# Performance work log

Measured on AMD Instinct MI355X. Metric: run time of the kernel, lower is better.

Reference implementation:

```python
import jax, jax.numpy as jnp
import numpy as np

N_NODES = 50000
N_EDGES = 800000
N_RELS = 65
D = 64
N_GRAPHS = 512


def setup_inputs() -> dict:
    key = jax.random.key(0)
    ks = jax.random.split(key, 20)
    inp = {
        "node_feats": jax.random.normal(ks[0], (N_NODES, D), dtype=jnp.float32),
        "etypes": jax.random.randint(ks[1], (N_EDGES,), 0, N_RELS),
        "src": jax.random.randint(ks[2], (N_EDGES,), 0, N_NODES),
        "dst": jax.random.randint(ks[3], (N_EDGES,), 0, N_NODES),
        "graph_ids": jnp.sort(jax.random.randint(ks[4], (N_NODES,), 0, N_GRAPHS)),
    }
    s = 1.0 / np.sqrt(D)
    # 3 RGCN layers: per-relation weights (basis with num_bases=num_rels == full) + bias
    for i, k in zip(range(1, 4), (ks[5], ks[6], ks[7])):
        inp[f"W_rel{i}"] = jax.random.normal(k, (N_RELS, D, D), dtype=jnp.float32) * s
        inp[f"b{i}"] = jnp.zeros((D,), dtype=jnp.float32)
    # 3 FC layers
    for i, k in zip(range(1, 4), (ks[8], ks[9], ks[10])):
        inp[f"fc_W{i}"] = jax.random.normal(k, (D, D), dtype=jnp.float32) * s
        inp[f"fc_b{i}"] = jnp.zeros((D,), dtype=jnp.float32)
    inp["pred_W"] = jax.random.normal(ks[11], (D, 2), dtype=jnp.float32) * s
    inp["pred_b"] = jnp.zeros((2,), dtype=jnp.float32)
    return inp


def _rgcn_layer(h, W, b, etypes, src, dst):
    # all-relation projection: [N, R, K]
    proj = jnp.einsum('nd,rdk->nrk', h, W)
    # per-edge gather of relation-specific message: [E, K]
    msg = proj[src, etypes]
    # scatter-sum into destination nodes
    agg = jax.ops.segment_sum(msg, dst, num_segments=h.shape[0])
    return jax.nn.relu(agg + b)


def reference(node_feats, etypes, src, dst, graph_ids,
              W_rel1, b1, W_rel2, b2, W_rel3, b3,
              fc_W1, fc_b1, fc_W2, fc_b2, fc_W3, fc_b3,
              pred_W, pred_b):
    h = node_feats
    h = _rgcn_layer(h, W_rel1, b1, etypes, src, dst)
    h = _rgcn_layer(h, W_rel2, b2, etypes, src, dst)
    h = _rgcn_layer(h, W_rel3, b3, etypes, src, dst)
    # sum-pool nodes per graph: [G, D]
    g = jax.ops.segment_sum(h, graph_ids, num_segments=N_GRAPHS)
    g = jax.nn.relu(g @ fc_W1 + fc_b1)
    g = jax.nn.relu(g @ fc_W2 + fc_b2)
    g = jax.nn.relu(g @ fc_W3 + fc_b3)
    return g @ pred_W + pred_b
```

## Files before the change

kernel.cpp:

```cpp
#include <hip/hip_runtime.h>
#include <hip/hip_bf16.h>

#define N_NODES 50000
#define N_EDGES 800000
#define N_RELS 65
#define DIM 64
#define N_GRAPHS 512

#define SORT_BLOCKS 1024
#define CHUNK ((N_EDGES + SORT_BLOCKS - 1) / SORT_BLOCKS)

#define SCAN_BLK 512
#define NSCAN_BLKS ((N_NODES + SCAN_BLK - 1) / SCAN_BLK)

#define MSG_BLOCKS 2048
#define NWAVES (MSG_BLOCKS * 4)

typedef __attribute__((ext_vector_type(8))) short short8;
typedef __attribute__((ext_vector_type(4))) float f32x4;


__global__ __launch_bounds__(256) void prep_kernel(
    const float* __restrict__ x, const int* __restrict__ et,
    __hip_bfloat16* __restrict__ y, int* __restrict__ cnt_d,
    int* __restrict__ blk_hist,
    const float* __restrict__ W1, const float* __restrict__ W2,
    const float* __restrict__ W3,
    __hip_bfloat16* __restrict__ Wt1, __hip_bfloat16* __restrict__ Wt2,
    __hip_bfloat16* __restrict__ Wt3,
    int* __restrict__ done_flags) {
    __shared__ int lh[N_RELS];
    __shared__ float tile[64][65];
    int t = threadIdx.x, b = blockIdx.x;
    int gtid = b * 256 + t;

    if (gtid < N_NODES) cnt_d[gtid] = 0;
    if (gtid < 2) done_flags[gtid] = 0;

    if (t < N_RELS) lh[t] = 0;
    __syncthreads();
    int lo = b * CHUNK;
    int hi = lo + CHUNK; if (hi > N_EDGES) hi = N_EDGES;
    for (int i = lo + t; i < hi; i += 256)
        atomicAdd(&lh[et[i]], 1);

    for (int i = gtid; i < (N_NODES * DIM) / 4; i += SORT_BLOCKS * 256) {
        float4 v = *(const float4*)(x + (size_t)i * 4);
        unsigned short us[4];
        us[0] = __hip_bfloat16_raw(__float2bfloat16(v.x)).x;
        us[1] = __hip_bfloat16_raw(__float2bfloat16(v.y)).x;
        us[2] = __hip_bfloat16_raw(__float2bfloat16(v.z)).x;
        us[3] = __hip_bfloat16_raw(__float2bfloat16(v.w)).x;
        *(ushort4*)(y + (size_t)i * 4) = *(const ushort4*)us;
    }

    if (b < 3 * N_RELS) {
        int which = b / N_RELS, r = b - which * N_RELS;
        const float* W = (which == 0) ? W1 : (which == 1) ? W2 : W3;
        __hip_bfloat16* Wt = (which == 0) ? Wt1 : (which == 1) ? Wt2 : Wt3;
        for (int i = t; i < 4096; i += 256) {
            int row = i >> 6, col = i & 63;
            tile[row][col] = W[(size_t)r * 4096 + i];
        }
        __syncthreads();
        for (int i = t; i < 4096; i += 256) {
            int row = i >> 6, col = i & 63;
            Wt[(size_t)r * 4096 + i] = __float2bfloat16(tile[col][row]);
        }
    }

    __syncthreads();
    if (t < N_RELS) blk_hist[t * SORT_BLOCKS + b] = lh[t];
}


__global__ __launch_bounds__(256) void relscan_kernel(const int* __restrict__ blk_hist,
                                                      int* __restrict__ blk_off,
                                                      int* __restrict__ rel_tot,
                                                      int* __restrict__ rel_ptr,
                                                      int* __restrict__ tile_base,
                                                      int* __restrict__ done) {
    __shared__ int wsum[4];
    int r = blockIdx.x;
    int t = threadIdx.x;
    int w = t >> 6, lane = t & 63;
    const int PER = SORT_BLOCKS / 256;
    int4 v0 = *(const int4*)(blk_hist + (size_t)r * SORT_BLOCKS + t * PER);
    int vals[4] = {v0.x, v0.y, v0.z, v0.w};
    int s = 0;
    #pragma unroll
    for (int j = 0; j < PER; ++j) s += vals[j];
    int x = s;
    #pragma unroll
    for (int off = 1; off < 64; off <<= 1) {
        int y = __shfl_up(x, off);
        if (lane >= off) x += y;
    }
    if (lane == 63) wsum[w] = x;
    __syncthreads();
    int base = 0;
    for (int i = 0; i < w; ++i) base += wsum[i];
    int run = base + x - s;
    int out[4];
    #pragma unroll
    for (int j = 0; j < PER; ++j) { out[j] = run; run += vals[j]; }
    *(int4*)(blk_off + (size_t)r * SORT_BLOCKS + t * PER) = *(const int4*)&out[0];

    if (t == 255) {
        __hip_atomic_store(&rel_tot[r], base + x, __ATOMIC_RELAXED, __HIP_MEMORY_SCOPE_AGENT);
        __threadfence();
        int ticket = atomicAdd(done, 1);
        if (ticket == N_RELS - 1) {
            int ss = 0, tt = 0;
            for (int q = 0; q < N_RELS; ++q) {
                int v = __hip_atomic_load(&rel_tot[q], __ATOMIC_RELAXED,
                                          __HIP_MEMORY_SCOPE_AGENT);
                rel_ptr[q] = ss; ss += v;
                tile_base[q] = tt; tt += (v + 15) >> 4;
            }
            rel_ptr[N_RELS] = N_EDGES;
            tile_base[N_RELS] = tt;
        }
    }
}


__global__ __launch_bounds__(256) void scatter2_kernel(
    const int* __restrict__ et, const int* __restrict__ src,
    const int* __restrict__ dst, const int* __restrict__ blk_hist,
    const int* __restrict__ blk_off, const int* __restrict__ rel_ptr,
    unsigned long long* __restrict__ epk, int* __restrict__ cnt_d) {
    __shared__ unsigned long long buf[CHUNK];
    __shared__ unsigned char relof[CHUNK];
    __shared__ int loff[N_RELS + 1];
    __shared__ int lcur[N_RELS];
    __shared__ int gbase[N_RELS];
    int t = threadIdx.x, b = blockIdx.x;

    if (t < 64) {
        int v = blk_hist[t * SORT_BLOCKS + b];
        int x = v;
        #pragma unroll
        for (int off = 1; off < 64; off <<= 1) {
            int y = __shfl_up(x, off);
            if (t >= off) x += y;
        }
        loff[t] = x - v;
        lcur[t] = x - v;
        gbase[t] = rel_ptr[t] + blk_off[t * SORT_BLOCKS + b];
        if (t == 63) { loff[64] = x; lcur[64] = x; }
    } else if (t == 64) {
        gbase[64] = rel_ptr[64] + blk_off[64 * SORT_BLOCKS + b];
    }
    __syncthreads();

    int lo = b * CHUNK;
    int hi = lo + CHUNK; if (hi > N_EDGES) hi = N_EDGES;
    int nloc = hi - lo;

    #pragma unroll
    for (int k = 0; k < 4; ++k) {
        int i = lo + t + k * 256;
        if (i < hi) {
            int r = et[i], d = dst[i];
            unsigned s = (unsigned)src[i];
            int rank = atomicAdd(&cnt_d[d], 1);
            int pl = atomicAdd(&lcur[r], 1);
            unsigned lo32 = s | ((unsigned)d << 16);
            buf[pl] = (unsigned long long)lo32 |
                      ((unsigned long long)(unsigned)rank << 32);
            relof[pl] = (unsigned char)r;
        }
    }
    __syncthreads();

    #pragma unroll
    for (int k = 0; k < 4; ++k) {
        int i = t + k * 256;
        if (i < nloc) {
            int r = relof[i];
            epk[gbase[r] + i - loff[r]] = buf[i];
        }
    }
}


__global__ __launch_bounds__(SCAN_BLK) void scanblk_kernel(
    const int* __restrict__ cnt, int* __restrict__ outv,
    int* __restrict__ blk_tot, int* __restrict__ blk_base,
    const int* __restrict__ gid, int* __restrict__ g_ptr,
    int* __restrict__ cnt_g, int* __restrict__ done) {
    __shared__ int tmp[SCAN_BLK];
    __shared__ int is_last;
    int t = threadIdx.x;
    int i = blockIdx.x * SCAN_BLK + t;
    int v = (i < N_NODES) ? cnt[i] : 0;
    tmp[t] = v;
    __syncthreads();
    for (int off = 1; off < SCAN_BLK; off <<= 1) {
        int add = (t >= off) ? tmp[t - off] : 0;
        __syncthreads();
        tmp[t] += add;
        __syncthreads();
    }
    if (i < N_NODES) outv[i] = tmp[t] - v;
    if (t == SCAN_BLK - 1) {
        __hip_atomic_store(&blk_tot[blockIdx.x], tmp[t], __ATOMIC_RELAXED,
                           __HIP_MEMORY_SCOPE_AGENT);
        __threadfence();
        int ticket = atomicAdd(done, 1);
        is_last = (ticket == NSCAN_BLKS - 1) ? 1 : 0;
    }
    __syncthreads();
    if (is_last) {
        if (t == 0) {
            int run = 0;
            for (int b2 = 0; b2 < NSCAN_BLKS; ++b2) {
                int v2 = __hip_atomic_load(&blk_tot[b2], __ATOMIC_RELAXED,
                                           __HIP_MEMORY_SCOPE_AGENT);
                blk_base[b2] = run; run += v2;
            }
        }
        if (t < N_GRAPHS) {
            int g = t;
            int lo2 = 0, hi2 = N_NODES;
            while (lo2 < hi2) { int m = (lo2 + hi2) >> 1; if (gid[m] < g) lo2 = m + 1; else hi2 = m; }
            int a2 = lo2;
            lo2 = 0; hi2 = N_NODES;
            int g1 = g + 1;
            while (lo2 < hi2) { int m = (lo2 + hi2) >> 1; if (gid[m] < g1) lo2 = m + 1; else hi2 = m; }
            g_ptr[g] = a2;
            cnt_g[g] = lo2 - a2;
        }
    }
}


__device__ inline unsigned pack2bf(float x, float y) {
    unsigned short ux = __hip_bfloat16_raw(__float2bfloat16(x)).x;
    unsigned short uy = __hip_bfloat16_raw(__float2bfloat16(y)).x;
    return (unsigned)ux | ((unsigned)uy << 16);
}

__global__ __launch_bounds__(256) void msg_mfma_kernel(
    const __hip_bfloat16* __restrict__ hb, const __hip_bfloat16* __restrict__ Wt,
    const int* __restrict__ rel_ptr, const int* __restrict__ tile_base,
    const unsigned long long* __restrict__ epk, const int* __restrict__ outv,
    const int* __restrict__ blk_base,
    __hip_bfloat16* __restrict__ msg) {
    int t = threadIdx.x;
    int w = t >> 6, lane = t & 63;
    int quad = lane >> 4, m16 = lane & 15;
    int wave = blockIdx.x * 4 + w;

    int ntiles = tile_base[N_RELS];
    int tpw = (ntiles + NWAVES - 1) / NWAVES;
    int T = wave * tpw;
    int T1 = T + tpw; if (T1 > ntiles) T1 = ntiles;
    if (T >= T1) return;

    int r = 0;
    while (T >= tile_base[r + 1]) ++r;

    while (T < T1) {
        int chunk_end = tile_base[r + 1]; if (chunk_end > T1) chunk_end = T1;
        int e_base = rel_ptr[r], t_base = tile_base[r];
        int seg_end = rel_ptr[r + 1];

        const __hip_bfloat16* Wr = Wt + (size_t)r * (DIM * DIM);
        short8 bf00 = *(const short8*)(Wr + (4 * m16)     * DIM + quad * 8);
        short8 bf01 = *(const short8*)(Wr + (4 * m16 + 1) * DIM + quad * 8);
        short8 bf02 = *(const short8*)(Wr + (4 * m16 + 2) * DIM + quad * 8);
        short8 bf03 = *(const short8*)(Wr + (4 * m16 + 3) * DIM + quad * 8);
        short8 bf10 = *(const short8*)(Wr + (4 * m16)     * DIM + 32 + quad * 8);
        short8 bf11 = *(const short8*)(Wr + (4 * m16 + 1) * DIM + 32 + quad * 8);
        short8 bf12 = *(const short8*)(Wr + (4 * m16 + 2) * DIM + 32 + quad * 8);
        short8 bf13 = *(const short8*)(Wr + (4 * m16 + 3) * DIM + 32 + quad * 8);

        auto loadidx = [&](int TT, int& sv, int& dp) {
            int TC = TT < chunk_end ? TT : chunk_end - 1;
            int i = e_base + (TC - t_base) * 16 + lane;
            if (i >= N_EDGES) i = N_EDGES - 1;
            unsigned long long e = epk[i];
            int d = (int)((e >> 16) & 0xFFFFu);
            sv = (int)(e & 0xFFFFu);
            dp = (int)(e >> 32) + outv[d] + blk_base[d >> 9];
        };
        auto gatherA = [&](int sv, short8& x0, short8& x1) {
            int s = __shfl(sv, m16);
            const __hip_bfloat16* hp = hb + (size_t)s * DIM + quad * 8;
            x0 = *(const short8*)hp;
            x1 = *(const short8*)(hp + 32);
        };

        int sv0, dp0, sv1, dp1, sv2, dp2;
        short8 a0c, a1c, a0n, a1n;
        loadidx(T,     sv0, dp0);
        loadidx(T + 1, sv1, dp1);
        gatherA(sv0, a0c, a1c);

        for (; T < chunk_end; ++T) {
            loadidx(T + 2, sv2, dp2);
            gatherA(sv1, a0n, a1n);

            int e0 = e_base + (T - t_base) * 16;
            int rows = seg_end - e0; if (rows > 16) rows = 16;

            f32x4 c0 = {0.f, 0.f, 0.f, 0.f}, c1 = c0, c2 = c0, c3 = c0;
            c0 = __builtin_amdgcn_mfma_f32_16x16x32_bf16(a0c, bf00, c0, 0, 0, 0);
            c1 = __builtin_amdgcn_mfma_f32_16x16x32_bf16(a0c, bf01, c1, 0, 0, 0);
            c2 = __builtin_amdgcn_mfma_f32_16x16x32_bf16(a0c, bf02, c2, 0, 0, 0);
            c3 = __builtin_amdgcn_mfma_f32_16x16x32_bf16(a0c, bf03, c3, 0, 0, 0);
            c0 = __builtin_amdgcn_mfma_f32_16x16x32_bf16(a1c, bf10, c0, 0, 0, 0);
            c1 = __builtin_amdgcn_mfma_f32_16x16x32_bf16(a1c, bf11, c1, 0, 0, 0);
            c2 = __builtin_amdgcn_mfma_f32_16x16x32_bf16(a1c, bf12, c2, 0, 0, 0);
            c3 = __builtin_amdgcn_mfma_f32_16x16x32_bf16(a1c, bf13, c3, 0, 0, 0);

            int dpr[4];
            #pragma unroll
            for (int g = 0; g < 4; ++g) dpr[g] = __shfl(dp0, quad * 4 + g);

            #pragma unroll
            for (int g = 0; g < 4; ++g) {
                if (quad * 4 + g < rows) {
                    uint2 pk;
                    pk.x = pack2bf(c0[g], c1[g]);
                    pk.y = pack2bf(c2[g], c3[g]);
                    *(uint2*)(msg + (size_t)dpr[g] * DIM + 4 * m16) = pk;
                }
            }

            sv0 = sv1; dp0 = dp1; sv1 = sv2; dp1 = dp2;
            a0c = a0n; a1c = a1n;
        }
        ++r;
        while (T < T1 && T >= tile_base[r + 1]) ++r;
    }
}


__global__ __launch_bounds__(256) void agg_kernel(
    const __hip_bfloat16* __restrict__ msg, const int* __restrict__ outv,
    const int* __restrict__ blk_base,
    const int* __restrict__ cnt_d, const float* __restrict__ b,
    __hip_bfloat16* __restrict__ hout) {
    int wave = blockIdx.x * 4 + (threadIdx.x >> 6);
    int lane = threadIdx.x & 63;
    if (wave >= N_NODES) return;
    int j0 = outv[wave] + blk_base[wave >> 9];
    int n  = cnt_d[wave];
    int rgrp = lane >> 3, dgrp = lane & 7;

    float a[8] = {0.f, 0.f, 0.f, 0.f, 0.f, 0.f, 0.f, 0.f};
    for (int jj = 0; jj < n; jj += 8) {
        int row = jj + rgrp;
        if (row < n) {
            uint4 d = *(const uint4*)(msg + (size_t)(j0 + row) * DIM + dgrp * 8);
            a[0] += __uint_as_float(d.x << 16);
            a[1] += __uint_as_float(d.x & 0xffff0000u);
            a[2] += __uint_as_float(d.y << 16);
            a[3] += __uint_as_float(d.y & 0xffff0000u);
            a[4] += __uint_as_float(d.z << 16);
            a[5] += __uint_as_float(d.z & 0xffff0000u);
            a[6] += __uint_as_float(d.w << 16);
            a[7] += __uint_as_float(d.w & 0xffff0000u);
        }
    }
    #pragma unroll
    for (int i = 0; i < 8; ++i) {
        a[i] += __shfl_xor(a[i], 8);
        a[i] += __shfl_xor(a[i], 16);
        a[i] += __shfl_xor(a[i], 32);
    }
    if (rgrp == 0) {
        unsigned short us[8];
        #pragma unroll
        for (int i = 0; i < 8; ++i) {
            float v = a[i] + b[dgrp * 8 + i];
            us[i] = __hip_bfloat16_raw(__float2bfloat16(v > 0.f ? v : 0.f)).x;
        }
        *(uint4*)(hout + (size_t)wave * DIM + dgrp * 8) = *(const uint4*)us;
    }
}


__global__ __launch_bounds__(256) void poolfc_kernel(
    const __hip_bfloat16* __restrict__ h, const int* __restrict__ g_ptr,
    const int* __restrict__ cnt_g,
    const float* __restrict__ W1, const float* __restrict__ b1,
    const float* __restrict__ W2, const float* __restrict__ b2,
    const float* __restrict__ W3, const float* __restrict__ b3,
    const float* __restrict__ pW, const float* __restrict__ pb,
    float* __restrict__ out) {
    int wave = blockIdx.x * 4 + (threadIdx.x >> 6);
    int lane = threadIdx.x & 63;
    if (wave >= N_GRAPHS) return;
    int j0 = g_ptr[wave];
    int n  = cnt_g[wave];
    int rgrp = lane >> 3, dgrp = lane & 7;

    float a[8] = {0.f, 0.f, 0.f, 0.f, 0.f, 0.f, 0.f, 0.f};
    for (int jj = 0; jj < n; jj += 8) {
        int row = jj + rgrp;
        if (row < n) {
            uint4 d = *(const uint4*)(h + (size_t)(j0 + row) * DIM + dgrp * 8);
            a[0] += __uint_as_float(d.x << 16);
            a[1] += __uint_as_float(d.x & 0xffff0000u);
            a[2] += __uint_as_float(d.y << 16);
            a[3] += __uint_as_float(d.y & 0xffff0000u);
            a[4] += __uint_as_float(d.z << 16);
            a[5] += __uint_as_float(d.z & 0xffff0000u);
            a[6] += __uint_as_float(d.w << 16);
            a[7] += __uint_as_float(d.w & 0xffff0000u);
        }
    }
    #pragma unroll
    for (int i = 0; i < 8; ++i) {
        a[i] += __shfl_xor(a[i], 8);
        a[i] += __shfl_xor(a[i], 16);
        a[i] += __shfl_xor(a[i], 32);
    }
    float v;
    {
        float acc = b1[lane];
        #pragma unroll
        for (int o = 0; o < 8; ++o)
            #pragma unroll
            for (int q = 0; q < 8; ++q)
                acc += __shfl(a[o], q) * W1[(q * 8 + o) * DIM + lane];
        v = acc > 0.f ? acc : 0.f;
    }
    {
        float acc = b2[lane];
        #pragma unroll
        for (int d = 0; d < DIM; ++d)
            acc += __shfl(v, d) * W2[d * DIM + lane];
        v = acc > 0.f ? acc : 0.f;
    }
    {
        float acc = b3[lane];
        #pragma unroll
        for (int d = 0; d < DIM; ++d)
            acc += __shfl(v, d) * W3[d * DIM + lane];
        v = acc > 0.f ? acc : 0.f;
    }
    float p0 = v * pW[lane * 2 + 0];
    float p1 = v * pW[lane * 2 + 1];
    #pragma unroll
    for (int off = 32; off > 0; off >>= 1) {
        p0 += __shfl_down(p0, off);
        p1 += __shfl_down(p1, off);
    }
    if (lane == 0) {
        out[wave * 2 + 0] = p0 + pb[0];
        out[wave * 2 + 1] = p1 + pb[1];
    }
}


extern "C" void kernel_launch(void* const* d_in, const int* in_sizes, int n_in,
                              void* d_out, int out_size, void* d_ws, size_t ws_size,
                              hipStream_t stream) {
    const float* node_feats = (const float*)d_in[0];
    const int*   etypes     = (const int*)d_in[1];
    const int*   src        = (const int*)d_in[2];
    const int*   dst        = (const int*)d_in[3];
    const int*   graph_ids  = (const int*)d_in[4];
    const float* W1 = (const float*)d_in[5];
    const float* b1 = (const float*)d_in[6];
    const float* W2 = (const float*)d_in[7];
    const float* b2 = (const float*)d_in[8];
    const float* W3 = (const float*)d_in[9];
    const float* b3 = (const float*)d_in[10];
    const float* fcW1 = (const float*)d_in[11];
    const float* fcb1 = (const float*)d_in[12];
    const float* fcW2 = (const float*)d_in[13];
    const float* fcb2 = (const float*)d_in[14];
    const float* fcW3 = (const float*)d_in[15];
    const float* fcb3 = (const float*)d_in[16];
    const float* pW = (const float*)d_in[17];
    const float* pb = (const float*)d_in[18];
    float* out = (float*)d_out;

    char* p = (char*)d_ws;
    auto alloc = [&](size_t bytes) -> void* {
        void* r = (void*)p;
        p += (bytes + 255) & ~(size_t)255;
        return r;
    };
    int* blk_hist  = (int*)alloc((size_t)SORT_BLOCKS * N_RELS * sizeof(int));
    int* blk_off   = (int*)alloc((size_t)SORT_BLOCKS * N_RELS * sizeof(int));
    int* rel_ptr   = (int*)alloc((N_RELS + 1) * sizeof(int));
    int* rel_tot   = (int*)alloc(N_RELS * sizeof(int));
    int* tile_base = (int*)alloc((N_RELS + 1) * sizeof(int));
    unsigned long long* epk = (unsigned long long*)alloc((size_t)N_EDGES * sizeof(unsigned long long));
    int* cnt_d     = (int*)alloc((size_t)N_NODES * sizeof(int));
    int* outv      = (int*)alloc((size_t)N_NODES * sizeof(int));
    int* blk_tot   = (int*)alloc(NSCAN_BLKS * sizeof(int));
    int* blk_base  = (int*)alloc(NSCAN_BLKS * sizeof(int));
    int* cnt_g     = (int*)alloc(N_GRAPHS * sizeof(int));
    int* g_ptr     = (int*)alloc(N_GRAPHS * sizeof(int));
    int* done_flags= (int*)alloc(2 * sizeof(int));
    __hip_bfloat16* hb0 = (__hip_bfloat16*)alloc((size_t)N_NODES * DIM * sizeof(__hip_bfloat16));
    __hip_bfloat16* hb1 = (__hip_bfloat16*)alloc((size_t)N_NODES * DIM * sizeof(__hip_bfloat16));
    __hip_bfloat16* Wt1 = (__hip_bfloat16*)alloc((size_t)N_RELS * DIM * DIM * sizeof(__hip_bfloat16));
    __hip_bfloat16* Wt2 = (__hip_bfloat16*)alloc((size_t)N_RELS * DIM * DIM * sizeof(__hip_bfloat16));
    __hip_bfloat16* Wt3 = (__hip_bfloat16*)alloc((size_t)N_RELS * DIM * DIM * sizeof(__hip_bfloat16));
    __hip_bfloat16* msg = (__hip_bfloat16*)alloc((size_t)N_EDGES * DIM * sizeof(__hip_bfloat16));

    const int AGG_BLOCKS = (N_NODES + 3) / 4;

    prep_kernel<<<SORT_BLOCKS, 256, 0, stream>>>(node_feats, etypes, hb0, cnt_d, blk_hist,
                                                 W1, W2, W3, Wt1, Wt2, Wt3, done_flags);
    relscan_kernel<<<N_RELS, 256, 0, stream>>>(blk_hist, blk_off, rel_tot,
                                               rel_ptr, tile_base, &done_flags[0]);
    scatter2_kernel<<<SORT_BLOCKS, 256, 0, stream>>>(etypes, src, dst, blk_hist, blk_off,
                                                     rel_ptr, epk, cnt_d);
    scanblk_kernel<<<NSCAN_BLKS, SCAN_BLK, 0, stream>>>(cnt_d, outv, blk_tot, blk_base,
                                                        graph_ids, g_ptr, cnt_g,
                                                        &done_flags[1]);

    msg_mfma_kernel<<<MSG_BLOCKS, 256, 0, stream>>>(hb0, Wt1, rel_ptr, tile_base,
                                                    epk, outv, blk_base, msg);
    agg_kernel<<<AGG_BLOCKS, 256, 0, stream>>>(msg, outv, blk_base, cnt_d, b1, hb1);

    msg_mfma_kernel<<<MSG_BLOCKS, 256, 0, stream>>>(hb1, Wt2, rel_ptr, tile_base,
                                                    epk, outv, blk_base, msg);
    agg_kernel<<<AGG_BLOCKS, 256, 0, stream>>>(msg, outv, blk_base, cnt_d, b2, hb0);

    msg_mfma_kernel<<<MSG_BLOCKS, 256, 0, stream>>>(hb0, Wt3, rel_ptr, tile_base,
                                                    epk, outv, blk_base, msg);
    agg_kernel<<<AGG_BLOCKS, 256, 0, stream>>>(msg, outv, blk_base, cnt_d, b3, hb1);

    poolfc_kernel<<<(N_GRAPHS + 3) / 4, 256, 0, stream>>>(hb1, g_ptr, cnt_g,
                                                          fcW1, fcb1, fcW2, fcb2,
                                                          fcW3, fcb3, pW, pb, out);
}
```

Baseline: 391.6 us.

## Replace global atomic dst counting with two-level chunked dst sort then relation scatter

The edge preprocessing now bins edges by destination chunk (512 nodes), sorts each chunk locally in shared memory to build a CSR row_ptr and per-dst counts, then scatters the edges into relation order. The message slot for each edge is therefore its dst-sorted position, so the slot assignment comes from deterministic local sorting rather than per-edge global atomicAdd ranks plus an outv/blk_base lookup. This removes 800k contended global atomics and the extra indirection in msg_mfma and agg. In exchange there are more preprocessing launches and extra passes over the edge arrays.

Result: faster. 369.1 us (-5.8%).

```diff
diff --git a/kernel.cpp b/kernel.cpp
--- a/kernel.cpp
+++ b/kernel.cpp
@@ -7,11 +7,10 @@
 #define DIM 64
 #define N_GRAPHS 512
 
-#define SORT_BLOCKS 1024
-#define CHUNK ((N_EDGES + SORT_BLOCKS - 1) / SORT_BLOCKS)
-
-#define SCAN_BLK 512
-#define NSCAN_BLKS ((N_NODES + SCAN_BLK - 1) / SCAN_BLK)
+#define DCH 512
+#define NCH 98
+#define SB3 256
+#define EC3 3125
 
 #define MSG_BLOCKS 2048
 #define NWAVES (MSG_BLOCKS * 4)
@@ -21,30 +20,32 @@
 
 
 __global__ __launch_bounds__(256) void prep_kernel(
-    const float* __restrict__ x, const int* __restrict__ et,
-    __hip_bfloat16* __restrict__ y, int* __restrict__ cnt_d,
-    int* __restrict__ blk_hist,
+    const float* __restrict__ x, const int* __restrict__ dst,
+    __hip_bfloat16* __restrict__ y, int* __restrict__ blk_hist3,
     const float* __restrict__ W1, const float* __restrict__ W2,
     const float* __restrict__ W3,
     __hip_bfloat16* __restrict__ Wt1, __hip_bfloat16* __restrict__ Wt2,
     __hip_bfloat16* __restrict__ Wt3,
     int* __restrict__ done_flags) {
-    __shared__ int lh[N_RELS];
+    __shared__ int chist[128];
     __shared__ float tile[64][65];
     int t = threadIdx.x, b = blockIdx.x;
     int gtid = b * 256 + t;
 
-    if (gtid < N_NODES) cnt_d[gtid] = 0;
     if (gtid < 2) done_flags[gtid] = 0;
 
-    if (t < N_RELS) lh[t] = 0;
-    __syncthreads();
-    int lo = b * CHUNK;
-    int hi = lo + CHUNK; if (hi > N_EDGES) hi = N_EDGES;
-    for (int i = lo + t; i < hi; i += 256)
-        atomicAdd(&lh[et[i]], 1);
-
-    for (int i = gtid; i < (N_NODES * DIM) / 4; i += SORT_BLOCKS * 256) {
+    if (b < SB3) {
+        if (t < 128) chist[t] = 0;
+        __syncthreads();
+        int lo = b * EC3;
+        #pragma unroll
+        for (int k = 0; k < 13; ++k) {
+            int i = lo + t + k * 256;
+            if (i < lo + EC3) atomicAdd(&chist[dst[i] >> 9], 1);
+        }
+    }
+
+    for (int i = gtid; i < (N_NODES * DIM) / 4; i += 1024 * 256) {
         float4 v = *(const float4*)(x + (size_t)i * 4);
         unsigned short us[4];
         us[0] = __hip_bfloat16_raw(__float2bfloat16(v.x)).x;
@@ -54,8 +55,9 @@
         *(ushort4*)(y + (size_t)i * 4) = *(const ushort4*)us;
     }
 
-    if (b < 3 * N_RELS) {
-        int which = b / N_RELS, r = b - which * N_RELS;
+    if (b >= SB3 && b < SB3 + 3 * N_RELS) {
+        int bb = b - SB3;
+        int which = bb / N_RELS, r = bb - which * N_RELS;
         const float* W = (which == 0) ? W1 : (which == 1) ? W2 : W3;
         __hip_bfloat16* Wt = (which == 0) ? Wt1 : (which == 1) ? Wt2 : Wt3;
         for (int i = t; i < 4096; i += 256) {
@@ -69,28 +71,25 @@
         }
     }
 
-    __syncthreads();
-    if (t < N_RELS) blk_hist[t * SORT_BLOCKS + b] = lh[t];
-}
-
-
-__global__ __launch_bounds__(256) void relscan_kernel(const int* __restrict__ blk_hist,
-                                                      int* __restrict__ blk_off,
-                                                      int* __restrict__ rel_tot,
-                                                      int* __restrict__ rel_ptr,
-                                                      int* __restrict__ tile_base,
-                                                      int* __restrict__ done) {
+    if (b < SB3) {
+        __syncthreads();
+        if (t < NCH) blk_hist3[t * SB3 + b] = chist[t];
+    }
+}
+
+
+__global__ __launch_bounds__(256) void chunkscan_kernel(
+    const int* __restrict__ blk_hist3, int* __restrict__ blk_off3,
+    int* __restrict__ chunk_tot, int* __restrict__ chunk_ptr,
+    const int* __restrict__ gid, int* __restrict__ g_ptr, int* __restrict__ cnt_g,
+    int* __restrict__ done) {
     __shared__ int wsum[4];
-    int r = blockIdx.x;
-    int t = threadIdx.x;
+    __shared__ int is_last;
+    int r = blockIdx.x, t = threadIdx.x;
     int w = t >> 6, lane = t & 63;
-    const int PER = SORT_BLOCKS / 256;
-    int4 v0 = *(const int4*)(blk_hist + (size_t)r * SORT_BLOCKS + t * PER);
-    int vals[4] = {v0.x, v0.y, v0.z, v0.w};
-    int s = 0;
-    #pragma unroll
-    for (int j = 0; j < PER; ++j) s += vals[j];
-    int x = s;
+
+    int v = blk_hist3[r * SB3 + t];
+    int x = v;
     #pragma unroll
     for (int off = 1; off < 64; off <<= 1) {
         int y = __shfl_up(x, off);
@@ -100,129 +99,28 @@
     __syncthreads();
     int base = 0;
     for (int i = 0; i < w; ++i) base += wsum[i];
-    int run = base + x - s;
-    int out[4];
-    #pragma unroll
-    for (int j = 0; j < PER; ++j) { out[j] = run; run += vals[j]; }
-    *(int4*)(blk_off + (size_t)r * SORT_BLOCKS + t * PER) = *(const int4*)&out[0];
+    blk_off3[r * SB3 + t] = base + x - v;
 
     if (t == 255) {
-        __hip_atomic_store(&rel_tot[r], base + x, __ATOMIC_RELAXED, __HIP_MEMORY_SCOPE_AGENT);
-        __threadfence();
-        int ticket = atomicAdd(done, 1);
-        if (ticket == N_RELS - 1) {
-            int ss = 0, tt = 0;
-            for (int q = 0; q < N_RELS; ++q) {
-                int v = __hip_atomic_load(&rel_tot[q], __ATOMIC_RELAXED,
-                                          __HIP_MEMORY_SCOPE_AGENT);
-                rel_ptr[q] = ss; ss += v;
-                tile_base[q] = tt; tt += (v + 15) >> 4;
-            }
-            rel_ptr[N_RELS] = N_EDGES;
-            tile_base[N_RELS] = tt;
-        }
-    }
-}
-
-
-__global__ __launch_bounds__(256) void scatter2_kernel(
-    const int* __restrict__ et, const int* __restrict__ src,
-    const int* __restrict__ dst, const int* __restrict__ blk_hist,
-    const int* __restrict__ blk_off, const int* __restrict__ rel_ptr,
-    unsigned long long* __restrict__ epk, int* __restrict__ cnt_d) {
-    __shared__ unsigned long long buf[CHUNK];
-    __shared__ unsigned char relof[CHUNK];
-    __shared__ int loff[N_RELS + 1];
-    __shared__ int lcur[N_RELS];
-    __shared__ int gbase[N_RELS];
-    int t = threadIdx.x, b = blockIdx.x;
-
-    if (t < 64) {
-        int v = blk_hist[t * SORT_BLOCKS + b];
-        int x = v;
-        #pragma unroll
-        for (int off = 1; off < 64; off <<= 1) {
-            int y = __shfl_up(x, off);
-            if (t >= off) x += y;
-        }
-        loff[t] = x - v;
-        lcur[t] = x - v;
-        gbase[t] = rel_ptr[t] + blk_off[t * SORT_BLOCKS + b];
-        if (t == 63) { loff[64] = x; lcur[64] = x; }
-    } else if (t == 64) {
-        gbase[64] = rel_ptr[64] + blk_off[64 * SORT_BLOCKS + b];
-    }
-    __syncthreads();
-
-    int lo = b * CHUNK;
-    int hi = lo + CHUNK; if (hi > N_EDGES) hi = N_EDGES;
-    int nloc = hi - lo;
-
-    #pragma unroll
-    for (int k = 0; k < 4; ++k) {
-        int i = lo + t + k * 256;
-        if (i < hi) {
-            int r = et[i], d = dst[i];
-            unsigned s = (unsigned)src[i];
-            int rank = atomicAdd(&cnt_d[d], 1);
-            int pl = atomicAdd(&lcur[r], 1);
-            unsigned lo32 = s | ((unsigned)d << 16);
-            buf[pl] = (unsigned long long)lo32 |
-                      ((unsigned long long)(unsigned)rank << 32);
-            relof[pl] = (unsigned char)r;
-        }
-    }
-    __syncthreads();
-
-    #pragma unroll
-    for (int k = 0; k < 4; ++k) {
-        int i = t + k * 256;
-        if (i < nloc) {
-            int r = relof[i];
-            epk[gbase[r] + i - loff[r]] = buf[i];
-        }
-    }
-}
-
-
-__global__ __launch_bounds__(SCAN_BLK) void scanblk_kernel(
-    const int* __restrict__ cnt, int* __restrict__ outv,
-    int* __restrict__ blk_tot, int* __restrict__ blk_base,
-    const int* __restrict__ gid, int* __restrict__ g_ptr,
-    int* __restrict__ cnt_g, int* __restrict__ done) {
-    __shared__ int tmp[SCAN_BLK];
-    __shared__ int is_last;
-    int t = threadIdx.x;
-    int i = blockIdx.x * SCAN_BLK + t;
-    int v = (i < N_NODES) ? cnt[i] : 0;
-    tmp[t] = v;
-    __syncthreads();
-    for (int off = 1; off < SCAN_BLK; off <<= 1) {
-        int add = (t >= off) ? tmp[t - off] : 0;
-        __syncthreads();
-        tmp[t] += add;
-        __syncthreads();
-    }
-    if (i < N_NODES) outv[i] = tmp[t] - v;
-    if (t == SCAN_BLK - 1) {
-        __hip_atomic_store(&blk_tot[blockIdx.x], tmp[t], __ATOMIC_RELAXED,
+        __hip_atomic_store(&chunk_tot[r], base + x, __ATOMIC_RELAXED,
                            __HIP_MEMORY_SCOPE_AGENT);
         __threadfence();
         int ticket = atomicAdd(done, 1);
-        is_last = (ticket == NSCAN_BLKS - 1) ? 1 : 0;
-    }
-    __syncthreads();
+        is_last = (ticket == NCH - 1) ? 1 : 0;
+    }
+    __syncthreads();
+
     if (is_last) {
         if (t == 0) {
             int run = 0;
-            for (int b2 = 0; b2 < NSCAN_BLKS; ++b2) {
-                int v2 = __hip_atomic_load(&blk_tot[b2], __ATOMIC_RELAXED,
+            for (int q = 0; q < NCH; ++q) {
+                int vv = __hip_atomic_load(&chunk_tot[q], __ATOMIC_RELAXED,
                                            __HIP_MEMORY_SCOPE_AGENT);
-                blk_base[b2] = run; run += v2;
+                chunk_ptr[q] = run; run += vv;
             }
-        }
-        if (t < N_GRAPHS) {
-            int g = t;
+            chunk_ptr[NCH] = run;
+        }
+        for (int g = t; g < N_GRAPHS; g += 256) {
             int lo2 = 0, hi2 = N_NODES;
             while (lo2 < hi2) { int m = (lo2 + hi2) >> 1; if (gid[m] < g) lo2 = m + 1; else hi2 = m; }
             int a2 = lo2;
@@ -236,6 +134,181 @@
 }
 
 
+__global__ __launch_bounds__(256) void scatterc_kernel(
+    const int* __restrict__ et, const int* __restrict__ src,
+    const int* __restrict__ dst, const int* __restrict__ blk_hist3,
+    const int* __restrict__ blk_off3, const int* __restrict__ chunk_ptr,
+    unsigned* __restrict__ epk2) {
+    __shared__ unsigned srec[EC3];
+    __shared__ unsigned char sbin[EC3];
+    __shared__ int loff[NCH], lcur[NCH], gbase[NCH];
+    __shared__ int wsum[4];
+    int t = threadIdx.x, b = blockIdx.x;
+    int w = t >> 6, lane = t & 63;
+
+    int v = (t < NCH) ? blk_hist3[t * SB3 + b] : 0;
+    int x = v;
+    #pragma unroll
+    for (int off = 1; off < 64; off <<= 1) {
+        int y = __shfl_up(x, off);
+        if (lane >= off) x += y;
+    }
+    if (lane == 63) wsum[w] = x;
+    __syncthreads();
+    int base = 0;
+    for (int i = 0; i < w; ++i) base += wsum[i];
+    if (t < NCH) {
+        int pref = base + x - v;
+        loff[t] = pref;
+        lcur[t] = pref;
+        gbase[t] = chunk_ptr[t] + blk_off3[t * SB3 + b];
+    }
+    __syncthreads();
+
+    int lo = b * EC3;
+    #pragma unroll
+    for (int k = 0; k < 13; ++k) {
+        int i = lo + t + k * 256;
+        if (i < lo + EC3) {
+            int d = dst[i];
+            int bin = d >> 9;
+            unsigned rec = (unsigned)src[i] | ((unsigned)(d & 511) << 16) |
+                           ((unsigned)et[i] << 25);
+            int pl = atomicAdd(&lcur[bin], 1);
+            srec[pl] = rec;
+            sbin[pl] = (unsigned char)bin;
+        }
+    }
+    __syncthreads();
+
+    #pragma unroll
+    for (int k = 0; k < 13; ++k) {
+        int i = t + k * 256;
+        if (i < EC3) {
+            int bin = sbin[i];
+            epk2[gbase[bin] + i - loff[bin]] = srec[i];
+        }
+    }
+}
+
+
+__global__ __launch_bounds__(256) void chunksort_kernel(
+    const unsigned* __restrict__ epk2, const int* __restrict__ chunk_ptr,
+    unsigned* __restrict__ efin2, int* __restrict__ cnt_d,
+    int* __restrict__ row_ptr, int* __restrict__ relh_g) {
+    __shared__ int h512[DCH], off512[DCH], cur512[DCH];
+    __shared__ int relh[N_RELS];
+    __shared__ int wsum[4];
+    int c = blockIdx.x, t = threadIdx.x;
+    int w = t >> 6, lane = t & 63;
+    int e0 = chunk_ptr[c], e1 = chunk_ptr[c + 1];
+    int n = e1 - e0;
+
+    h512[2 * t] = 0; h512[2 * t + 1] = 0;
+    if (t < N_RELS) relh[t] = 0;
+    __syncthreads();
+
+    for (int i = t; i < n; i += 256) {
+        unsigned v = epk2[e0 + i];
+        atomicAdd(&h512[(v >> 16) & 511], 1);
+        atomicAdd(&relh[v >> 25], 1);
+    }
+    __syncthreads();
+
+    int v0 = h512[2 * t], v1 = h512[2 * t + 1];
+    int s = v0 + v1;
+    int x = s;
+    #pragma unroll
+    for (int off = 1; off < 64; off <<= 1) {
+        int y = __shfl_up(x, off);
+        if (lane >= off) x += y;
+    }
+    if (lane == 63) wsum[w] = x;
+    __syncthreads();
+    int base = 0;
+    for (int i = 0; i < w; ++i) base += wsum[i];
+    int run = base + x - s;
+    off512[2 * t] = run;
+    off512[2 * t + 1] = run + v0;
+    cur512[2 * t] = run;
+    cur512[2 * t + 1] = run + v0;
+    __syncthreads();
+
+    #pragma unroll
+    for (int j = t; j < DCH; j += 256) {
+        int d = c * DCH + j;
+        if (d < N_NODES) { cnt_d[d] = h512[j]; row_ptr[d] = e0 + off512[j]; }
+    }
+    if (t < N_RELS) relh_g[t * NCH + c] = relh[t];
+    __syncthreads();
+
+    for (int i = t; i < n; i += 256) {
+        unsigned v = epk2[e0 + i];
+        int dl = (v >> 16) & 511;
+        int pos = atomicAdd(&cur512[dl], 1);
+        efin2[e0 + pos] = (v & 0xFFFFu) | ((v >> 25) << 16);
+    }
+}
+
+
+__global__ __launch_bounds__(128) void relscan_kernel(
+    const int* __restrict__ relh_g, int* __restrict__ blk_off_rel,
+    int* __restrict__ rel_tot, int* __restrict__ rel_ptr,
+    int* __restrict__ tile_base, int* __restrict__ done) {
+    __shared__ int wsum2[2];
+    int r = blockIdx.x, t = threadIdx.x;
+    int w = t >> 6, lane = t & 63;
+    int v = (t < NCH) ? relh_g[r * NCH + t] : 0;
+    int x = v;
+    #pragma unroll
+    for (int off = 1; off < 64; off <<= 1) {
+        int y = __shfl_up(x, off);
+        if (lane >= off) x += y;
+    }
+    if (lane == 63) wsum2[w] = x;
+    __syncthreads();
+    int base = (w == 1) ? wsum2[0] : 0;
+    if (t < NCH) blk_off_rel[r * NCH + t] = base + x - v;
+
+    if (t == 127) {
+        int tot = wsum2[0] + wsum2[1];
+        __hip_atomic_store(&rel_tot[r], tot, __ATOMIC_RELAXED, __HIP_MEMORY_SCOPE_AGENT);
+        __threadfence();
+        int ticket = atomicAdd(done, 1);
+        if (ticket == N_RELS - 1) {
+            int ss = 0, tt = 0;
+            for (int q = 0; q < N_RELS; ++q) {
+                int vv = __hip_atomic_load(&rel_tot[q], __ATOMIC_RELAXED,
+                                           __HIP_MEMORY_SCOPE_AGENT);
+                rel_ptr[q] = ss; ss += vv;
+                tile_base[q] = tt; tt += (vv + 15) >> 4;
+            }
+            rel_ptr[N_RELS] = N_EDGES;
+            tile_base[N_RELS] = tt;
+        }
+    }
+}
+
+
+__global__ __launch_bounds__(256) void relscatter_kernel(
+    const unsigned* __restrict__ efin2, const int* __restrict__ chunk_ptr,
+    const int* __restrict__ rel_ptr, const int* __restrict__ blk_off_rel,
+    unsigned long long* __restrict__ epk3) {
+    __shared__ int lcur[N_RELS];
+    int c = blockIdx.x, t = threadIdx.x;
+    int e0 = chunk_ptr[c], n = chunk_ptr[c + 1] - e0;
+    if (t < N_RELS) lcur[t] = rel_ptr[t] + blk_off_rel[t * NCH + c];
+    __syncthreads();
+    for (int i = t; i < n; i += 256) {
+        unsigned v = efin2[e0 + i];
+        int rel = v >> 16;
+        int pos = atomicAdd(&lcur[rel], 1);
+        epk3[pos] = (unsigned long long)(v & 0xFFFFu) |
+                    ((unsigned long long)(unsigned)(e0 + i) << 32);
+    }
+}
+
+
 __device__ inline unsigned pack2bf(float x, float y) {
     unsigned short ux = __hip_bfloat16_raw(__float2bfloat16(x)).x;
     unsigned short uy = __hip_bfloat16_raw(__float2bfloat16(y)).x;
@@ -245,8 +318,7 @@
 __global__ __launch_bounds__(256) void msg_mfma_kernel(
     const __hip_bfloat16* __restrict__ hb, const __hip_bfloat16* __restrict__ Wt,
     const int* __restrict__ rel_ptr, const int* __restrict__ tile_base,
-    const unsigned long long* __restrict__ epk, const int* __restrict__ outv,
-    const int* __restrict__ blk_base,
+    const unsigned long long* __restrict__ epk3,
     __hip_bfloat16* __restrict__ msg) {
     int t = threadIdx.x;
     int w = t >> 6, lane = t & 63;
@@ -281,10 +353,9 @@
             int TC = TT < chunk_end ? TT : chunk_end - 1;
             int i = e_base + (TC - t_base) * 16 + lane;
             if (i >= N_EDGES) i = N_EDGES - 1;
-            unsigned long long e = epk[i];
-            int d = (int)((e >> 16) & 0xFFFFu);
+            unsigned long long e = epk3[i];
             sv = (int)(e & 0xFFFFu);
-            dp = (int)(e >> 32) + outv[d] + blk_base[d >> 9];
+            dp = (int)(e >> 32);
         };
         auto gatherA = [&](int sv, short8& x0, short8& x1) {
             int s = __shfl(sv, m16);
@@ -340,14 +411,13 @@
 
 
 __global__ __launch_bounds__(256) void agg_kernel(
-    const __hip_bfloat16* __restrict__ msg, const int* __restrict__ outv,
-    const int* __restrict__ blk_base,
+    const __hip_bfloat16* __restrict__ msg, const int* __restrict__ row_ptr,
     const int* __restrict__ cnt_d, const float* __restrict__ b,
     __hip_bfloat16* __restrict__ hout) {
     int wave = blockIdx.x * 4 + (threadIdx.x >> 6);
     int lane = threadIdx.x & 63;
     if (wave >= N_NODES) return;
-    int j0 = outv[wave] + blk_base[wave >> 9];
+    int j0 = row_ptr[wave];
     int n  = cnt_d[wave];
     int rgrp = lane >> 3, dgrp = lane & 7;
 
@@ -488,19 +558,23 @@
         p += (bytes + 255) & ~(size_t)255;
         return r;
     };
-    int* blk_hist  = (int*)alloc((size_t)SORT_BLOCKS * N_RELS * sizeof(int));
-    int* blk_off   = (int*)alloc((size_t)SORT_BLOCKS * N_RELS * sizeof(int));
-    int* rel_ptr   = (int*)alloc((N_RELS + 1) * sizeof(int));
-    int* rel_tot   = (int*)alloc(N_RELS * sizeof(int));
-    int* tile_base = (int*)alloc((N_RELS + 1) * sizeof(int));
-    unsigned long long* epk = (unsigned long long*)alloc((size_t)N_EDGES * sizeof(unsigned long long));
-    int* cnt_d     = (int*)alloc((size_t)N_NODES * sizeof(int));
-    int* outv      = (int*)alloc((size_t)N_NODES * sizeof(int));
-    int* blk_tot   = (int*)alloc(NSCAN_BLKS * sizeof(int));
-    int* blk_base  = (int*)alloc(NSCAN_BLKS * sizeof(int));
-    int* cnt_g     = (int*)alloc(N_GRAPHS * sizeof(int));
-    int* g_ptr     = (int*)alloc(N_GRAPHS * sizeof(int));
-    int* done_flags= (int*)alloc(2 * sizeof(int));
+    int* blk_hist3  = (int*)alloc((size_t)NCH * SB3 * sizeof(int));
+    int* blk_off3   = (int*)alloc((size_t)NCH * SB3 * sizeof(int));
+    int* chunk_tot  = (int*)alloc(NCH * sizeof(int));
+    int* chunk_ptr  = (int*)alloc((NCH + 1) * sizeof(int));
+    unsigned* epk2  = (unsigned*)alloc((size_t)N_EDGES * sizeof(unsigned));
+    unsigned* efin2 = (unsigned*)alloc((size_t)N_EDGES * sizeof(unsigned));
+    unsigned long long* epk3 = (unsigned long long*)alloc((size_t)N_EDGES * sizeof(unsigned long long));
+    int* relh_g     = (int*)alloc((size_t)N_RELS * NCH * sizeof(int));
+    int* blk_off_rel= (int*)alloc((size_t)N_RELS * NCH * sizeof(int));
+    int* rel_tot    = (int*)alloc(N_RELS * sizeof(int));
+    int* rel_ptr    = (int*)alloc((N_RELS + 1) * sizeof(int));
+    int* tile_base  = (int*)alloc((N_RELS + 1) * sizeof(int));
+    int* cnt_d      = (int*)alloc((size_t)N_NODES * sizeof(int));
+    int* row_ptr    = (int*)alloc((size_t)N_NODES * sizeof(int));
+    int* cnt_g      = (int*)alloc(N_GRAPHS * sizeof(int));
+    int* g_ptr      = (int*)alloc(N_GRAPHS * sizeof(int));
+    int* done_flags = (int*)alloc(2 * sizeof(int));
     __hip_bfloat16* hb0 = (__hip_bfloat16*)alloc((size_t)N_NODES * DIM * sizeof(__hip_bfloat16));
     __hip_bfloat16* hb1 = (__hip_bfloat16*)alloc((size_t)N_NODES * DIM * sizeof(__hip_bfloat16));
     __hip_bfloat16* Wt1 = (__hip_bfloat16*)alloc((size_t)N_RELS * DIM * DIM * sizeof(__hip_bfloat16));
@@ -510,27 +584,30 @@
 
     const int AGG_BLOCKS = (N_NODES + 3) / 4;
 
-    prep_kernel<<<SORT_BLOCKS, 256, 0, stream>>>(node_feats, etypes, hb0, cnt_d, blk_hist,
-                                                 W1, W2, W3, Wt1, Wt2, Wt3, done_flags);
-    relscan_kernel<<<N_RELS, 256, 0, stream>>>(blk_hist, blk_off, rel_tot,
-                                               rel_ptr, tile_base, &done_flags[0]);
-    scatter2_kernel<<<SORT_BLOCKS, 256, 0, stream>>>(etypes, src, dst, blk_hist, blk_off,
-                                                     rel_ptr, epk, cnt_d);
-    scanblk_kernel<<<NSCAN_BLKS, SCAN_BLK, 0, stream>>>(cnt_d, outv, blk_tot, blk_base,
-                                                        graph_ids, g_ptr, cnt_g,
-                                                        &done_flags[1]);
+    prep_kernel<<<1024, 256, 0, stream>>>(node_feats, dst, hb0, blk_hist3,
+                                          W1, W2, W3, Wt1, Wt2, Wt3, done_flags);
+    chunkscan_kernel<<<NCH, 256, 0, stream>>>(blk_hist3, blk_off3, chunk_tot, chunk_ptr,
+                                              graph_ids, g_ptr, cnt_g, &done_flags[0]);
+    scatterc_kernel<<<SB3, 256, 0, stream>>>(etypes, src, dst, blk_hist3, blk_off3,
+                                             chunk_ptr, epk2);
+    chunksort_kernel<<<NCH, 256, 0, stream>>>(epk2, chunk_ptr, efin2, cnt_d,
+                                              row_ptr, relh_g);
+    relscan_kernel<<<N_RELS, 128, 0, stream>>>(relh_g, blk_off_rel, rel_tot,
+                                               rel_ptr, tile_base, &done_flags[1]);
+    relscatter_kernel<<<NCH, 256, 0, stream>>>(efin2, chunk_ptr, rel_ptr,
+                                               blk_off_rel, epk3);
 
     msg_mfma_kernel<<<MSG_BLOCKS, 256, 0, stream>>>(hb0, Wt1, rel_ptr, tile_base,
-                                                    epk, outv, blk_base, msg);
-    agg_kernel<<<AGG_BLOCKS, 256, 0, stream>>>(msg, outv, blk_base, cnt_d, b1, hb1);
+                                                    epk3, msg);
+    agg_kernel<<<AGG_BLOCKS, 256, 0, stream>>>(msg, row_ptr, cnt_d, b1, hb1);
 
     msg_mfma_kernel<<<MSG_BLOCKS, 256, 0, stream>>>(hb1, Wt2, rel_ptr, tile_base,
-                                                    epk, outv, blk_base, msg);
-    agg_kernel<<<AGG_BLOCKS, 256, 0, stream>>>(msg, outv, blk_base, cnt_d, b2, hb0);
+                                                    epk3, msg);
+    agg_kernel<<<AGG_BLOCKS, 256, 0, stream>>>(msg, row_ptr, cnt_d, b2, hb0);
 
     msg_mfma_kernel<<<MSG_BLOCKS, 256, 0, stream>>>(hb0, Wt3, rel_ptr, tile_base,
-                                                    epk, outv, blk_base, msg);
-    agg_kernel<<<AGG_BLOCKS, 256, 0, stream>>>(msg, outv, blk_base, cnt_d, b3, hb1);
+                                                    epk3, msg);
+    agg_kernel<<<AGG_BLOCKS, 256, 0, stream>>>(msg, row_ptr, cnt_d, b3, hb1);
 
     poolfc_kernel<<<(N_GRAPHS + 3) / 4, 256, 0, stream>>>(hb1, g_ptr, cnt_g,
                                                           fcW1, fcb1, fcW2, fcb2,
```
